# Kernel tuning notes

Measured on AMD Instinct MI355X. Metric: run time of the kernel, lower is better.

## Reference

```python
import jax, jax.numpy as jnp
import numpy as np

IN_FEATURES = 1024
OUT_FEATURES = 1024
B, S = 8, 4096


def setup_inputs() -> dict:
    key = jax.random.key(0)
    kx, kw = jax.random.split(key)
    x = jax.random.normal(kx, (B, S, IN_FEATURES), dtype=jnp.float32)
    # weight initialized as randn * 0.1, shape [out_features, in_features]
    weight = jax.random.normal(kw, (OUT_FEATURES, IN_FEATURES), dtype=jnp.float32) * 0.1
    bias = jnp.zeros((OUT_FEATURES,), dtype=jnp.float32)
    return {"x": x, "weight": weight, "bias": bias}


def reference(x, weight, bias):
    # BitNetLinear eval-mode forward.
    # Weight quantization to ternary {-1, 0, +1} with mean-abs scale.
    w_scale = jnp.mean(jnp.abs(weight))  # scalar
    q_weight = jnp.sign(weight) * (jnp.abs(weight) > 0.5 * w_scale).astype(weight.dtype)
    # Activation quantization to int8 range with global abs-max scale.
    i_scale = jnp.max(jnp.abs(x)) / 127.0  # scalar
    q_input = jnp.clip(jnp.round(x / i_scale), -128.0, 127.0)
    # Float GEMM on quantized values, then dequant with both scales.
    out = jnp.einsum('bsk,ok->bso', q_input, q_weight) * w_scale * i_scale
    out = out + bias  # bias added after dequant, matching the torch code
    return out
```

## Files before the change

### kernel.cpp

```cpp
#include <hip/hip_runtime.h>
#include <stdint.h>


#define MK_M 32768
#define MK_K 1024
#define MK_N 1024

typedef __attribute__((ext_vector_type(4))) int int32x4;

#define WS_MAXP_OFF 64
#define WS_PART_OFF 8448
#define WS_QW_OFF 16384
#define WS_QX_OFF (16384 + (1 << 20))
#define WS_NEEDED (WS_QX_OFF + (size_t)MK_M * MK_K)

__global__ void kprep(const float4* __restrict__ x4, const float4* __restrict__ w4,
                      float* __restrict__ maxp, double* __restrict__ partials, long n4x) {
    const int bid = blockIdx.x;
    if (bid < 2048) {
        float m = 0.f;
        const long stride = 2048L * 256;
        for (long i = (long)bid * 256 + threadIdx.x; i < n4x; i += stride) {
            float4 v = x4[i];
            m = fmaxf(m, fmaxf(fmaxf(fabsf(v.x), fabsf(v.y)), fmaxf(fabsf(v.z), fabsf(v.w))));
        }
        #pragma unroll
        for (int off = 1; off < 64; off <<= 1) m = fmaxf(m, __shfl_xor(m, off));
        __shared__ float sm[4];
        int lane = threadIdx.x & 63, wid = threadIdx.x >> 6;
        if (lane == 0) sm[wid] = m;
        __syncthreads();
        if (threadIdx.x == 0) maxp[bid] = fmaxf(fmaxf(sm[0], sm[1]), fmaxf(sm[2], sm[3]));
    } else {
        double s = 0.0;
        for (int i = (bid - 2048) * 256 + threadIdx.x; i < (1 << 18); i += 64 * 256) {
            float4 v = w4[i];
            s += (double)fabsf(v.x);
            s += (double)fabsf(v.y);
            s += (double)fabsf(v.z);
            s += (double)fabsf(v.w);
        }
        __shared__ double sd[256];
        sd[threadIdx.x] = s;
        __syncthreads();
        for (int h = 128; h > 0; h >>= 1) {
            if ((int)threadIdx.x < h) sd[threadIdx.x] += sd[threadIdx.x + h];
            __syncthreads();
        }
        if (threadIdx.x == 0) partials[bid - 2048] = sd[0];
    }
}

__global__ void kquant_w(const float4* __restrict__ w4, unsigned* __restrict__ qw,
                         const double* __restrict__ partials, float* __restrict__ wscp) {
    __shared__ double sws;
    if (threadIdx.x < 64) {
        double s = partials[threadIdx.x];
        #pragma unroll
        for (int off = 1; off < 64; off <<= 1) s += __shfl_xor(s, off);
        if (threadIdx.x == 0) sws = s;
    }
    __syncthreads();
    float wsc = (float)(sws / 1048576.0);
    if (blockIdx.x == 0 && threadIdx.x == 0) *wscp = wsc;
    float thr = 0.5f * wsc;
    int stride = gridDim.x * blockDim.x;
    for (int i = blockIdx.x * blockDim.x + threadIdx.x; i < (1 << 18); i += stride) {
        float4 v = w4[i];
        int q0 = (fabsf(v.x) > thr) ? (v.x > 0.f ? 1 : -1) : 0;
        int q1 = (fabsf(v.y) > thr) ? (v.y > 0.f ? 1 : -1) : 0;
        int q2 = (fabsf(v.z) > thr) ? (v.z > 0.f ? 1 : -1) : 0;
        int q3 = (fabsf(v.w) > thr) ? (v.w > 0.f ? 1 : -1) : 0;
        qw[i] = (q0 & 0xff) | ((q1 & 0xff) << 8) | ((q2 & 0xff) << 16) | ((q3 & 0xff) << 24);
    }
}

__global__ void kquant_x(const float4* __restrict__ x4, unsigned* __restrict__ qx,
                         const float* __restrict__ maxp, float* __restrict__ iscp, long n4) {
    float m = 0.f;
    #pragma unroll
    for (int j = 0; j < 8; ++j) m = fmaxf(m, maxp[threadIdx.x + 256 * j]);
    #pragma unroll
    for (int off = 1; off < 64; off <<= 1) m = fmaxf(m, __shfl_xor(m, off));
    __shared__ float sm[4];
    int lane = threadIdx.x & 63, wid = threadIdx.x >> 6;
    if (lane == 0) sm[wid] = m;
    __syncthreads();
    float isc = fmaxf(fmaxf(sm[0], sm[1]), fmaxf(sm[2], sm[3])) / 127.0f;
    if (blockIdx.x == 0 && threadIdx.x == 0) *iscp = isc;
    long stride = (long)gridDim.x * blockDim.x;
    for (long i = (long)blockIdx.x * blockDim.x + threadIdx.x; i < n4; i += stride) {
        float4 v = x4[i];
        float q0 = fminf(fmaxf(rintf(v.x / isc), -128.f), 127.f);
        float q1 = fminf(fmaxf(rintf(v.y / isc), -128.f), 127.f);
        float q2 = fminf(fmaxf(rintf(v.z / isc), -128.f), 127.f);
        float q3 = fminf(fmaxf(rintf(v.w / isc), -128.f), 127.f);
        int i0 = (int)q0, i1 = (int)q1, i2 = (int)q2, i3 = (int)q3;
        qx[i] = (i0 & 0xff) | ((i1 & 0xff) << 8) | ((i2 & 0xff) << 16) | ((i3 & 0xff) << 24);
    }
}

__global__ __launch_bounds__(256, 3) void kgemm(
    const char* __restrict__ qx, const char* __restrict__ qw,
    const float* __restrict__ bias, const float* __restrict__ wscp,
    const float* __restrict__ iscp, float* __restrict__ out)
{
    __shared__ __align__(16) char smem[3 * 16384];

    const int t = threadIdx.x;
    const int l = t & 63;
    const int w = t >> 6;
    const int wm = w >> 1;
    const int wn = w & 1;

    const int bid = blockIdx.x;
    const int wg = (bid & 7) * 256 + (bid >> 3);
    const int tm = wg >> 3, tn = wg & 7;
    const long m0 = (long)tm * 128;
    const int n0 = tn * 128;

    const int grow = t >> 2;
    const int gch = (t & 3) ^ ((t >> 3) & 3);
    const char* gAt = qx + (m0 + grow) * (long)MK_K + gch * 16;
    const char* gBt = qw + (long)(n0 + grow) * MK_K + gch * 16;

    auto stage = [&](int kt1, int b) {
        char* dst = smem + b * 16384 + t * 16;
        const char* sa = gAt + kt1 * 64;
        const char* sb = gBt + kt1 * 64;
        __builtin_amdgcn_global_load_lds(
            (const __attribute__((address_space(1))) void*)sa,
            (__attribute__((address_space(3))) void*)dst, 16, 0, 0);
        __builtin_amdgcn_global_load_lds(
            (const __attribute__((address_space(1))) void*)(sa + 64 * (long)MK_K),
            (__attribute__((address_space(3))) void*)(dst + 4096), 16, 0, 0);
        __builtin_amdgcn_global_load_lds(
            (const __attribute__((address_space(1))) void*)sb,
            (__attribute__((address_space(3))) void*)(dst + 8192), 16, 0, 0);
        __builtin_amdgcn_global_load_lds(
            (const __attribute__((address_space(1))) void*)(sb + 64 * (long)MK_K),
            (__attribute__((address_space(3))) void*)(dst + 12288), 16, 0, 0);
    };

    int32x4 acc[4][4];
    #pragma unroll
    for (int mi = 0; mi < 4; ++mi)
        #pragma unroll
        for (int ni = 0; ni < 4; ++ni) acc[mi][ni] = (int32x4)0;

    stage(0, 0);
    stage(1, 1);

    #pragma unroll
    for (int kt = 0; kt < 16; ++kt) {
        if (kt < 15) asm volatile("s_waitcnt vmcnt(4)" ::: "memory");
        else         asm volatile("s_waitcnt vmcnt(0)" ::: "memory");
        __builtin_amdgcn_s_barrier();

        const char* bufA = smem + (kt % 3) * 16384;
        const char* bufB = bufA + 8192;

        int32x4 af[4], bf[4];
        #pragma unroll
        for (int i = 0; i < 4; ++i) {
            int row = wm * 64 + i * 16 + (l & 15);
            int ch = (l >> 4) ^ ((row >> 1) & 3);
            af[i] = *(const int32x4*)(bufA + row * 64 + ch * 16);
        }
        #pragma unroll
        for (int i = 0; i < 4; ++i) {
            int row = wn * 64 + i * 16 + (l & 15);
            int ch = (l >> 4) ^ ((row >> 1) & 3);
            bf[i] = *(const int32x4*)(bufB + row * 64 + ch * 16);
        }
        if (kt < 14) stage(kt + 2, (kt + 2) % 3);
        __builtin_amdgcn_s_setprio(1);
        #pragma unroll
        for (int mi = 0; mi < 4; ++mi)
            #pragma unroll
            for (int ni = 0; ni < 4; ++ni)
                acc[mi][ni] = __builtin_amdgcn_mfma_i32_16x16x64_i8(
                    af[mi], bf[ni], acc[mi][ni], 0, 0, 0);
        __builtin_amdgcn_s_setprio(0);
    }

    const float wsc = *wscp, isc = *iscp;
    const int crow = (l >> 4) * 4;
    const int ccol = l & 15;
    #pragma unroll
    for (int mi = 0; mi < 4; ++mi) {
        #pragma unroll
        for (int ni = 0; ni < 4; ++ni) {
            long r0 = m0 + wm * 64 + mi * 16 + crow;
            int c = n0 + wn * 64 + ni * 16 + ccol;
            float b = bias[c];
            #pragma unroll
            for (int j = 0; j < 4; ++j) {
                out[(r0 + j) * MK_N + c] = ((float)acc[mi][ni][j] * wsc) * isc + b;
            }
        }
    }
}

extern "C" void kernel_launch(void* const* d_in, const int* in_sizes, int n_in,
                              void* d_out, int out_size, void* d_ws, size_t ws_size,
                              hipStream_t stream) {
    const float* x = (const float*)d_in[0];
    const float* wt = (const float*)d_in[1];
    const float* bias = (const float*)d_in[2];
    float* out = (float*)d_out;

    if (ws_size < WS_NEEDED) return;

    char* ws = (char*)d_ws;
    float* wscp = (float*)(ws + 0);
    float* iscp = (float*)(ws + 4);
    float* maxp = (float*)(ws + WS_MAXP_OFF);
    double* partials = (double*)(ws + WS_PART_OFF);
    char* qw = ws + WS_QW_OFF;
    char* qx = ws + WS_QX_OFF;

    const long n_x = (long)in_sizes[0];
    const long n4_x = n_x >> 2;

    kprep<<<2112, 256, 0, stream>>>((const float4*)x, (const float4*)wt, maxp, partials, n4_x);
    kquant_w<<<256, 256, 0, stream>>>((const float4*)wt, (unsigned*)qw, partials, wscp);
    kquant_x<<<2048, 256, 0, stream>>>((const float4*)x, (unsigned*)qx, maxp, iscp, n4_x);

    const int grid = (MK_M / 128) * (MK_N / 128);
    kgemm<<<grid, 256, 0, stream>>>(qx, qw, bias, wscp, iscp, out);
}
```

Measured before the change: 110.6 us.

## Fuse activation quantization into GEMM with full-K LDS row tiles

Removes the separate kquant_x pass and the int8 qx buffer. Each block now quantizes 64 full rows of x straight into a 64KB swizzled LDS tile, then computes all 1024 output columns by looping over N chunks, with each wave streaming its own weight fragments from global memory into registers under software double-buffering. This avoids writing and re-reading 32MB of int8 activations and drops one kernel launch. In exchange, weight reuse across waves is lost because B is read per wave with no LDS sharing, occupancy is lower due to the 64KB LDS use, and the GEMM phase cannot overlap the quantize phase within a block.

After: 123.3 us. 11.5% more time.

```diff
diff --git a/kernel.cpp b/kernel.cpp
--- a/kernel.cpp
+++ b/kernel.cpp
@@ -11,8 +11,7 @@
 #define WS_MAXP_OFF 64
 #define WS_PART_OFF 8448
 #define WS_QW_OFF 16384
-#define WS_QX_OFF (16384 + (1 << 20))
-#define WS_NEEDED (WS_QX_OFF + (size_t)MK_M * MK_K)
+#define WS_NEEDED (WS_QW_OFF + (1 << 20))
 
 __global__ void kprep(const float4* __restrict__ x4, const float4* __restrict__ w4,
                       float* __restrict__ maxp, double* __restrict__ partials, long n4x) {
@@ -75,128 +74,122 @@
     }
 }
 
-__global__ void kquant_x(const float4* __restrict__ x4, unsigned* __restrict__ qx,
-                         const float* __restrict__ maxp, float* __restrict__ iscp, long n4) {
-    float m = 0.f;
-    #pragma unroll
-    for (int j = 0; j < 8; ++j) m = fmaxf(m, maxp[threadIdx.x + 256 * j]);
-    #pragma unroll
-    for (int off = 1; off < 64; off <<= 1) m = fmaxf(m, __shfl_xor(m, off));
+__global__ __launch_bounds__(256, 2) void kfused(
+    const float* __restrict__ x, const char* __restrict__ qw,
+    const float* __restrict__ bias, const float* __restrict__ wscp,
+    const float* __restrict__ maxp, float* __restrict__ out)
+{
+    __shared__ __align__(16) char qa[64 * 1024];
     __shared__ float sm[4];
-    int lane = threadIdx.x & 63, wid = threadIdx.x >> 6;
-    if (lane == 0) sm[wid] = m;
-    __syncthreads();
-    float isc = fmaxf(fmaxf(sm[0], sm[1]), fmaxf(sm[2], sm[3])) / 127.0f;
-    if (blockIdx.x == 0 && threadIdx.x == 0) *iscp = isc;
-    long stride = (long)gridDim.x * blockDim.x;
-    for (long i = (long)blockIdx.x * blockDim.x + threadIdx.x; i < n4; i += stride) {
-        float4 v = x4[i];
-        float q0 = fminf(fmaxf(rintf(v.x / isc), -128.f), 127.f);
-        float q1 = fminf(fmaxf(rintf(v.y / isc), -128.f), 127.f);
-        float q2 = fminf(fmaxf(rintf(v.z / isc), -128.f), 127.f);
-        float q3 = fminf(fmaxf(rintf(v.w / isc), -128.f), 127.f);
-        int i0 = (int)q0, i1 = (int)q1, i2 = (int)q2, i3 = (int)q3;
-        qx[i] = (i0 & 0xff) | ((i1 & 0xff) << 8) | ((i2 & 0xff) << 16) | ((i3 & 0xff) << 24);
-    }
-}
-
-__global__ __launch_bounds__(256, 3) void kgemm(
-    const char* __restrict__ qx, const char* __restrict__ qw,
-    const float* __restrict__ bias, const float* __restrict__ wscp,
-    const float* __restrict__ iscp, float* __restrict__ out)
-{
-    __shared__ __align__(16) char smem[3 * 16384];
 
     const int t = threadIdx.x;
     const int l = t & 63;
     const int w = t >> 6;
-    const int wm = w >> 1;
-    const int wn = w & 1;
-
-    const int bid = blockIdx.x;
-    const int wg = (bid & 7) * 256 + (bid >> 3);
-    const int tm = wg >> 3, tn = wg & 7;
-    const long m0 = (long)tm * 128;
-    const int n0 = tn * 128;
-
-    const int grow = t >> 2;
-    const int gch = (t & 3) ^ ((t >> 3) & 3);
-    const char* gAt = qx + (m0 + grow) * (long)MK_K + gch * 16;
-    const char* gBt = qw + (long)(n0 + grow) * MK_K + gch * 16;
-
-    auto stage = [&](int kt1, int b) {
-        char* dst = smem + b * 16384 + t * 16;
-        const char* sa = gAt + kt1 * 64;
-        const char* sb = gBt + kt1 * 64;
-        __builtin_amdgcn_global_load_lds(
-            (const __attribute__((address_space(1))) void*)sa,
-            (__attribute__((address_space(3))) void*)dst, 16, 0, 0);
-        __builtin_amdgcn_global_load_lds(
-            (const __attribute__((address_space(1))) void*)(sa + 64 * (long)MK_K),
-            (__attribute__((address_space(3))) void*)(dst + 4096), 16, 0, 0);
-        __builtin_amdgcn_global_load_lds(
-            (const __attribute__((address_space(1))) void*)sb,
-            (__attribute__((address_space(3))) void*)(dst + 8192), 16, 0, 0);
-        __builtin_amdgcn_global_load_lds(
-            (const __attribute__((address_space(1))) void*)(sb + 64 * (long)MK_K),
-            (__attribute__((address_space(3))) void*)(dst + 12288), 16, 0, 0);
-    };
-
-    int32x4 acc[4][4];
+    const long m0 = (long)blockIdx.x * 64;
+
+    float m = 0.f;
     #pragma unroll
-    for (int mi = 0; mi < 4; ++mi)
-        #pragma unroll
-        for (int ni = 0; ni < 4; ++ni) acc[mi][ni] = (int32x4)0;
-
-    stage(0, 0);
-    stage(1, 1);
-
+    for (int j = 0; j < 8; ++j) m = fmaxf(m, maxp[t + 256 * j]);
     #pragma unroll
-    for (int kt = 0; kt < 16; ++kt) {
-        if (kt < 15) asm volatile("s_waitcnt vmcnt(4)" ::: "memory");
-        else         asm volatile("s_waitcnt vmcnt(0)" ::: "memory");
-        __builtin_amdgcn_s_barrier();
-
-        const char* bufA = smem + (kt % 3) * 16384;
-        const char* bufB = bufA + 8192;
-
-        int32x4 af[4], bf[4];
-        #pragma unroll
-        for (int i = 0; i < 4; ++i) {
-            int row = wm * 64 + i * 16 + (l & 15);
-            int ch = (l >> 4) ^ ((row >> 1) & 3);
-            af[i] = *(const int32x4*)(bufA + row * 64 + ch * 16);
-        }
-        #pragma unroll
-        for (int i = 0; i < 4; ++i) {
-            int row = wn * 64 + i * 16 + (l & 15);
-            int ch = (l >> 4) ^ ((row >> 1) & 3);
-            bf[i] = *(const int32x4*)(bufB + row * 64 + ch * 16);
-        }
-        if (kt < 14) stage(kt + 2, (kt + 2) % 3);
-        __builtin_amdgcn_s_setprio(1);
+    for (int off = 1; off < 64; off <<= 1) m = fmaxf(m, __shfl_xor(m, off));
+    if (l == 0) sm[w] = m;
+    __syncthreads();
+    const float isc = fmaxf(fmaxf(sm[0], sm[1]), fmaxf(sm[2], sm[3])) / 127.0f;
+    const float rin = 1.0f / isc;
+
+    for (int j = 0; j < 16; ++j) {
+        const int row = w * 16 + j;
+        const float4* src = (const float4*)(x + (m0 + row) * MK_K);
+        #pragma unroll
+        for (int e = 0; e < 4; ++e) {
+            float4 v = src[e * 64 + l];
+            int i0 = (int)fminf(fmaxf(rintf(v.x * rin), -128.f), 127.f);
+            int i1 = (int)fminf(fmaxf(rintf(v.y * rin), -128.f), 127.f);
+            int i2 = (int)fminf(fmaxf(rintf(v.z * rin), -128.f), 127.f);
+            int i3 = (int)fminf(fmaxf(rintf(v.w * rin), -128.f), 127.f);
+            unsigned pk = (i0 & 0xff) | ((i1 & 0xff) << 8) | ((i2 & 0xff) << 16) | ((i3 & 0xff) << 24);
+            const int d = e * 64 + l;
+            const int dsw = ((((d >> 2) ^ (row & 7)) << 2) | (d & 3));
+            *(unsigned*)(qa + row * 1024 + dsw * 4) = pk;
+        }
+    }
+    __syncthreads();
+
+    const float wsc = *wscp;
+    const int crow = (l >> 4) * 4;
+    const int ccol = l & 15;
+
+    for (int nc = 0; nc < 4; ++nc) {
+        const int nb = w * 256 + nc * 64;
+        const char* bq = qw + (long)(nb + (l & 15)) * MK_K + (l >> 4) * 16;
+
+        int32x4 acc[4][4];
         #pragma unroll
         for (int mi = 0; mi < 4; ++mi)
             #pragma unroll
-            for (int ni = 0; ni < 4; ++ni)
-                acc[mi][ni] = __builtin_amdgcn_mfma_i32_16x16x64_i8(
-                    af[mi], bf[ni], acc[mi][ni], 0, 0, 0);
-        __builtin_amdgcn_s_setprio(0);
-    }
-
-    const float wsc = *wscp, isc = *iscp;
-    const int crow = (l >> 4) * 4;
-    const int ccol = l & 15;
-    #pragma unroll
-    for (int mi = 0; mi < 4; ++mi) {
-        #pragma unroll
-        for (int ni = 0; ni < 4; ++ni) {
-            long r0 = m0 + wm * 64 + mi * 16 + crow;
-            int c = n0 + wn * 64 + ni * 16 + ccol;
-            float b = bias[c];
+            for (int ni = 0; ni < 4; ++ni) acc[mi][ni] = (int32x4)0;
+
+        int32x4 bfP[4], bfQ[4];
+        #pragma unroll
+        for (int i = 0; i < 4; ++i)
+            bfP[i] = *(const int32x4*)(bq + i * 16 * MK_K);
+
+        #pragma unroll 2
+        for (int kp = 0; kp < 8; ++kp) {
+            {
+                const int kt = 2 * kp;
+                int32x4 af[4];
+                #pragma unroll
+                for (int i = 0; i < 4; ++i) {
+                    int row = i * 16 + (l & 15);
+                    int cc = (kt * 4 + (l >> 4)) ^ (row & 7);
+                    af[i] = *(const int32x4*)(qa + row * 1024 + cc * 16);
+                }
+                #pragma unroll
+                for (int i = 0; i < 4; ++i)
+                    bfQ[i] = *(const int32x4*)(bq + i * 16 * MK_K + (kt + 1) * 64);
+                #pragma unroll
+                for (int mi = 0; mi < 4; ++mi)
+                    #pragma unroll
+                    for (int ni = 0; ni < 4; ++ni)
+                        acc[mi][ni] = __builtin_amdgcn_mfma_i32_16x16x64_i8(
+                            af[mi], bfP[ni], acc[mi][ni], 0, 0, 0);
+            }
+            {
+                const int kt = 2 * kp + 1;
+                int32x4 af[4];
+                #pragma unroll
+                for (int i = 0; i < 4; ++i) {
+                    int row = i * 16 + (l & 15);
+                    int cc = (kt * 4 + (l >> 4)) ^ (row & 7);
+                    af[i] = *(const int32x4*)(qa + row * 1024 + cc * 16);
+                }
+                if (kt < 15) {
+                    #pragma unroll
+                    for (int i = 0; i < 4; ++i)
+                        bfP[i] = *(const int32x4*)(bq + i * 16 * MK_K + (kt + 1) * 64);
+                }
+                #pragma unroll
+                for (int mi = 0; mi < 4; ++mi)
+                    #pragma unroll
+                    for (int ni = 0; ni < 4; ++ni)
+                        acc[mi][ni] = __builtin_amdgcn_mfma_i32_16x16x64_i8(
+                            af[mi], bfQ[ni], acc[mi][ni], 0, 0, 0);
+            }
+        }
+
+        const float s2 = wsc * 1.0f;
+        #pragma unroll
+        for (int mi = 0; mi < 4; ++mi) {
             #pragma unroll
-            for (int j = 0; j < 4; ++j) {
-                out[(r0 + j) * MK_N + c] = ((float)acc[mi][ni][j] * wsc) * isc + b;
+            for (int ni = 0; ni < 4; ++ni) {
+                long r0 = m0 + mi * 16 + crow;
+                int c = nb + ni * 16 + ccol;
+                float b = bias[c];
+                #pragma unroll
+                for (int j = 0; j < 4; ++j) {
+                    out[(r0 + j) * MK_N + c] = ((float)acc[mi][ni][j] * s2) * isc + b;
+                }
             }
         }
     }
@@ -214,19 +207,14 @@
 
     char* ws = (char*)d_ws;
     float* wscp = (float*)(ws + 0);
-    float* iscp = (float*)(ws + 4);
     float* maxp = (float*)(ws + WS_MAXP_OFF);
     double* partials = (double*)(ws + WS_PART_OFF);
     char* qw = ws + WS_QW_OFF;
-    char* qx = ws + WS_QX_OFF;
 
     const long n_x = (long)in_sizes[0];
     const long n4_x = n_x >> 2;
 
     kprep<<<2112, 256, 0, stream>>>((const float4*)x, (const float4*)wt, maxp, partials, n4_x);
     kquant_w<<<256, 256, 0, stream>>>((const float4*)wt, (unsigned*)qw, partials, wscp);
-    kquant_x<<<2048, 256, 0, stream>>>((const float4*)x, (unsigned*)qx, maxp, iscp, n4_x);
-
-    const int grid = (MK_M / 128) * (MK_N / 128);
-    kgemm<<<grid, 256, 0, stream>>>(qx, qw, bias, wscp, iscp, out);
-}
+    kfused<<<MK_M / 64, 256, 0, stream>>>(x, qw, bias, wscp, maxp, out);
+}
```

## Fuse activation int8 quantization into the GEMM main loop

Applied to the files above, without the earlier changes.

Removes the separate kquant_x pass and the int8 activation buffer in workspace. The GEMM now loads fp32 x tiles into registers, quantizes them in-kernel using the global abs-max (reduced per block from the kprep partials), and writes packed int8 into a double-buffered LDS tile, while the weight tile still streams via global_load_lds with triple buffering. The tile grows to 128x256 with 512 threads so each fp32 activation tile is reused across more output columns. The intent is to avoid writing and re-reading the quantized activations. The cost is more fp32 traffic into the GEMM, extra register pressure, and a main loop that is no longer explicitly unrolled.

Result: faster. 103.2 us, median of 4 (-6.7%).

```diff
diff --git a/kernel.cpp b/kernel.cpp
--- a/kernel.cpp
+++ b/kernel.cpp
@@ -11,8 +11,7 @@
 #define WS_MAXP_OFF 64
 #define WS_PART_OFF 8448
 #define WS_QW_OFF 16384
-#define WS_QX_OFF (16384 + (1 << 20))
-#define WS_NEEDED (WS_QX_OFF + (size_t)MK_M * MK_K)
+#define WS_NEEDED (WS_QW_OFF + (1 << 20))
 
 __global__ void kprep(const float4* __restrict__ x4, const float4* __restrict__ w4,
                       float* __restrict__ maxp, double* __restrict__ partials, long n4x) {
@@ -75,91 +74,107 @@
     }
 }
 
-__global__ void kquant_x(const float4* __restrict__ x4, unsigned* __restrict__ qx,
-                         const float* __restrict__ maxp, float* __restrict__ iscp, long n4) {
-    float m = 0.f;
-    #pragma unroll
-    for (int j = 0; j < 8; ++j) m = fmaxf(m, maxp[threadIdx.x + 256 * j]);
-    #pragma unroll
-    for (int off = 1; off < 64; off <<= 1) m = fmaxf(m, __shfl_xor(m, off));
-    __shared__ float sm[4];
-    int lane = threadIdx.x & 63, wid = threadIdx.x >> 6;
-    if (lane == 0) sm[wid] = m;
-    __syncthreads();
-    float isc = fmaxf(fmaxf(sm[0], sm[1]), fmaxf(sm[2], sm[3])) / 127.0f;
-    if (blockIdx.x == 0 && threadIdx.x == 0) *iscp = isc;
-    long stride = (long)gridDim.x * blockDim.x;
-    for (long i = (long)blockIdx.x * blockDim.x + threadIdx.x; i < n4; i += stride) {
-        float4 v = x4[i];
-        float q0 = fminf(fmaxf(rintf(v.x / isc), -128.f), 127.f);
-        float q1 = fminf(fmaxf(rintf(v.y / isc), -128.f), 127.f);
-        float q2 = fminf(fmaxf(rintf(v.z / isc), -128.f), 127.f);
-        float q3 = fminf(fmaxf(rintf(v.w / isc), -128.f), 127.f);
-        int i0 = (int)q0, i1 = (int)q1, i2 = (int)q2, i3 = (int)q3;
-        qx[i] = (i0 & 0xff) | ((i1 & 0xff) << 8) | ((i2 & 0xff) << 16) | ((i3 & 0xff) << 24);
-    }
-}
-
-__global__ __launch_bounds__(256, 3) void kgemm(
-    const char* __restrict__ qx, const char* __restrict__ qw,
+__global__ __launch_bounds__(512, 2) void kfused(
+    const float* __restrict__ x, const char* __restrict__ qw,
     const float* __restrict__ bias, const float* __restrict__ wscp,
-    const float* __restrict__ iscp, float* __restrict__ out)
+    const float* __restrict__ maxp, float* __restrict__ out)
 {
-    __shared__ __align__(16) char smem[3 * 16384];
+    __shared__ __align__(16) char As[2][8192];
+    __shared__ __align__(16) char Bs[3][16384];
+    __shared__ float smx[8];
 
     const int t = threadIdx.x;
     const int l = t & 63;
     const int w = t >> 6;
-    const int wm = w >> 1;
-    const int wn = w & 1;
+    const int wm = w >> 2;
+    const int wn = w & 3;
 
     const int bid = blockIdx.x;
-    const int wg = (bid & 7) * 256 + (bid >> 3);
-    const int tm = wg >> 3, tn = wg & 7;
+    const int wg = (bid & 7) * 128 + (bid >> 3);
+    const int tm = wg >> 2, tn = wg & 3;
     const long m0 = (long)tm * 128;
-    const int n0 = tn * 128;
-
-    const int grow = t >> 2;
+    const int n0 = tn * 256;
+
+    float m = 0.f;
+    #pragma unroll
+    for (int j = 0; j < 4; ++j) m = fmaxf(m, maxp[t + 512 * j]);
+    #pragma unroll
+    for (int off = 1; off < 64; off <<= 1) m = fmaxf(m, __shfl_xor(m, off));
+    if (l == 0) smx[w] = m;
+    __syncthreads();
+    const float mm = fmaxf(fmaxf(fmaxf(smx[0], smx[1]), fmaxf(smx[2], smx[3])),
+                           fmaxf(fmaxf(smx[4], smx[5]), fmaxf(smx[6], smx[7])));
+    const float isc = mm / 127.0f;
+    const float rin = 1.0f / isc;
+
+    const int arow = t >> 2;
+    const int ac = t & 3;
+    const float4* gA4 = (const float4*)(x + (m0 + arow) * MK_K + ac * 16);
+    const int adsw = (ac ^ ((arow >> 1) & 3));
+    char* const adst0 = (char*)As[0] + arow * 64 + adsw * 16;
+    char* const adst1 = (char*)As[1] + arow * 64 + adsw * 16;
+
     const int gch = (t & 3) ^ ((t >> 3) & 3);
-    const char* gAt = qx + (m0 + grow) * (long)MK_K + gch * 16;
-    const char* gBt = qw + (long)(n0 + grow) * MK_K + gch * 16;
-
-    auto stage = [&](int kt1, int b) {
-        char* dst = smem + b * 16384 + t * 16;
-        const char* sa = gAt + kt1 * 64;
-        const char* sb = gBt + kt1 * 64;
+    const char* gBt = qw + ((long)n0 + (t >> 2)) * MK_K + gch * 16;
+    auto stageB = [&](int kt1, int b) {
+        char* dst = (char*)Bs[b] + t * 16;
+        const char* src = gBt + kt1 * 64;
         __builtin_amdgcn_global_load_lds(
-            (const __attribute__((address_space(1))) void*)sa,
+            (const __attribute__((address_space(1))) void*)src,
             (__attribute__((address_space(3))) void*)dst, 16, 0, 0);
         __builtin_amdgcn_global_load_lds(
-            (const __attribute__((address_space(1))) void*)(sa + 64 * (long)MK_K),
-            (__attribute__((address_space(3))) void*)(dst + 4096), 16, 0, 0);
-        __builtin_amdgcn_global_load_lds(
-            (const __attribute__((address_space(1))) void*)sb,
+            (const __attribute__((address_space(1))) void*)(src + 128L * MK_K),
             (__attribute__((address_space(3))) void*)(dst + 8192), 16, 0, 0);
-        __builtin_amdgcn_global_load_lds(
-            (const __attribute__((address_space(1))) void*)(sb + 64 * (long)MK_K),
-            (__attribute__((address_space(3))) void*)(dst + 12288), 16, 0, 0);
     };
 
+    float4 ar0, ar1, ar2, ar3;
+    auto issueA = [&](int kt1) {
+        ar0 = gA4[kt1 * 16 + 0];
+        ar1 = gA4[kt1 * 16 + 1];
+        ar2 = gA4[kt1 * 16 + 2];
+        ar3 = gA4[kt1 * 16 + 3];
+    };
+    auto quantA = [&](char* dst) {
+        int p[4];
+        float4 vv[4] = {ar0, ar1, ar2, ar3};
+        #pragma unroll
+        for (int q = 0; q < 4; ++q) {
+            int i0 = (int)rintf(vv[q].x * rin);
+            int i1 = (int)rintf(vv[q].y * rin);
+            int i2 = (int)rintf(vv[q].z * rin);
+            int i3 = (int)rintf(vv[q].w * rin);
+            p[q] = (i0 & 0xff) | ((i1 & 0xff) << 8) | ((i2 & 0xff) << 16) | ((i3 & 0xff) << 24);
+        }
+        int32x4 pk = {p[0], p[1], p[2], p[3]};
+        *(int32x4*)dst = pk;
+    };
+
     int32x4 acc[4][4];
     #pragma unroll
     for (int mi = 0; mi < 4; ++mi)
         #pragma unroll
         for (int ni = 0; ni < 4; ++ni) acc[mi][ni] = (int32x4)0;
 
-    stage(0, 0);
-    stage(1, 1);
-
-    #pragma unroll
+    issueA(0);
+    stageB(0, 0);
+    asm volatile("s_waitcnt vmcnt(2)" ::: "memory");
+    quantA(adst0);
+    issueA(1);
+    stageB(1, 1);
+
     for (int kt = 0; kt < 16; ++kt) {
-        if (kt < 15) asm volatile("s_waitcnt vmcnt(4)" ::: "memory");
-        else         asm volatile("s_waitcnt vmcnt(0)" ::: "memory");
+        if (kt < 15) asm volatile("s_waitcnt vmcnt(2) lgkmcnt(0)" ::: "memory");
+        else         asm volatile("s_waitcnt vmcnt(0) lgkmcnt(0)" ::: "memory");
         __builtin_amdgcn_s_barrier();
 
-        const char* bufA = smem + (kt % 3) * 16384;
-        const char* bufB = bufA + 8192;
-
+        if (kt < 15) quantA((kt & 1) ? adst0 : adst1);
+        if (kt < 14) {
+            issueA(kt + 2);
+            stageB(kt + 2, (kt + 2) % 3);
+        }
+
+        const char* bufA = As[kt & 1];
+        const char* bufB = Bs[kt % 3];
         int32x4 af[4], bf[4];
         #pragma unroll
         for (int i = 0; i < 4; ++i) {
@@ -173,7 +188,6 @@
             int ch = (l >> 4) ^ ((row >> 1) & 3);
             bf[i] = *(const int32x4*)(bufB + row * 64 + ch * 16);
         }
-        if (kt < 14) stage(kt + 2, (kt + 2) % 3);
         __builtin_amdgcn_s_setprio(1);
         #pragma unroll
         for (int mi = 0; mi < 4; ++mi)
@@ -184,7 +198,7 @@
         __builtin_amdgcn_s_setprio(0);
     }
 
-    const float wsc = *wscp, isc = *iscp;
+    const float wsc = *wscp;
     const int crow = (l >> 4) * 4;
     const int ccol = l & 15;
     #pragma unroll
@@ -214,19 +228,16 @@
 
     char* ws = (char*)d_ws;
     float* wscp = (float*)(ws + 0);
-    float* iscp = (float*)(ws + 4);
     float* maxp = (float*)(ws + WS_MAXP_OFF);
     double* partials = (double*)(ws + WS_PART_OFF);
     char* qw = ws + WS_QW_OFF;
-    char* qx = ws + WS_QX_OFF;
 
     const long n_x = (long)in_sizes[0];
     const long n4_x = n_x >> 2;
 
     kprep<<<2112, 256, 0, stream>>>((const float4*)x, (const float4*)wt, maxp, partials, n4_x);
     kquant_w<<<256, 256, 0, stream>>>((const float4*)wt, (unsigned*)qw, partials, wscp);
-    kquant_x<<<2048, 256, 0, stream>>>((const float4*)x, (unsigned*)qx, maxp, iscp, n4_x);
-
-    const int grid = (MK_M / 128) * (MK_N / 128);
-    kgemm<<<grid, 256, 0, stream>>>(qx, qw, bias, wscp, iscp, out);
-}
+
+    const int grid = (MK_M / 128) * (MK_N / 256);
+    kfused<<<grid, 512, 0, stream>>>(x, qw, bias, wscp, maxp, out);
+}
```
